# Performance work log

Hardware: AMD Instinct MI355X
Metric: run time of the kernel (lower is better)

Reference implementation:

```python
import jax, jax.numpy as jnp
import numpy as np

IN_FEATURES = 1024
OUT_FEATURES = 256
GRID_SIZE = 5
SPLINE_ORDER = 3
SCALE_BASE = 1.0
GRID_RANGE = (-1.0, 1.0)


def make_grid():
    h = (GRID_RANGE[1] - GRID_RANGE[0]) / GRID_SIZE
    g = jnp.arange(-SPLINE_ORDER, GRID_SIZE + SPLINE_ORDER + 1, dtype=jnp.float32) * h + GRID_RANGE[0]
    # (in_features, grid_size + 2*spline_order + 1) = (1024, 12)
    return jnp.broadcast_to(g[None, :], (IN_FEATURES, g.shape[0]))


def setup_inputs() -> dict:
    key = jax.random.key(0)
    k1, k2, k3 = jax.random.split(key, 3)
    batch = 16384
    x = jax.random.normal(k1, (batch, IN_FEATURES), dtype=jnp.float32)
    base_weight = jax.random.normal(k2, (OUT_FEATURES, IN_FEATURES), dtype=jnp.float32) * 0.03
    n_basis = GRID_SIZE + SPLINE_ORDER  # 8
    spline_weight = (jax.random.uniform(k3, (OUT_FEATURES, IN_FEATURES * n_basis), dtype=jnp.float32) - 0.5) * 0.1 / n_basis
    grid = make_grid()
    return {"x": x, "base_weight": base_weight, "spline_weight": spline_weight, "grid": grid}


def b_splines(x, grid):
    # x: (B, F) -> (B, F, grid_size + spline_order)
    xe = x[:, :, None]  # (B, F, 1)
    bases = ((xe >= grid[:, :-1]) & (xe < grid[:, 1:])).astype(x.dtype)
    for k in range(1, SPLINE_ORDER + 1):
        left = (xe - grid[:, : -(k + 1)]) / (grid[:, k:-1] - grid[:, : -(k + 1)])
        right = (grid[:, k + 1 :] - xe) / (grid[:, k + 1 :] - grid[:, 1:-k])
        bases = left * bases[:, :, :-1] + right * bases[:, :, 1:]
    return bases.reshape(x.shape[0], -1)  # (B, F*(grid_size+spline_order))


def reference(x, base_weight, spline_weight, grid):
    base_out = jax.nn.silu(x) @ (base_weight * SCALE_BASE).T  # (B, out)
    spline_basis = b_splines(x, grid)                          # (B, F*8)
    spline_out = spline_basis @ spline_weight.T                # (B, out)
    return base_out + spline_out
```

## Files before the change

kernel.cpp:

```cpp
#include <hip/hip_runtime.h>
#include <cstdint>
#include <cstddef>

typedef unsigned short u16;
typedef unsigned int   u32;
typedef unsigned long long u64;
typedef __attribute__((ext_vector_type(8))) short short8;
typedef __attribute__((ext_vector_type(4))) float f32x4;

#define M_ROWS 16384
#define N_COLS 256
#define IN_F   1024
#define K_SPL  8192
#define K_TOT  9216
#define NCHUNK 144
#define SPLITK 2
#define CPB    (NCHUNK / SPLITK)

__device__ __forceinline__ u32 f2bf1(float f) {
  u32 u = __float_as_uint(f);
  u += 0x7fffu + ((u >> 16) & 1u);
  return u >> 16;
}
__device__ __forceinline__ u32 pk2(float a, float b) {
  return f2bf1(a) | (f2bf1(b) << 16);
}
__device__ __forceinline__ float silu(float v) {
  return v * __builtin_amdgcn_rcpf(1.f + __expf(-v));
}

__device__ __forceinline__ uint4 basis8(float xv) {
  float u = fmaf(xv, 2.5f, 5.5f);
  int i0 = (int)u;
  float fr = u - (float)i0;
  float fr2 = fr * fr, fr3 = fr2 * fr;
  float om  = 1.f - fr;
  float om3 = om * om * om;
  float w0 = om3 * (1.f / 6.f);
  float w3 = fr3 * (1.f / 6.f);
  float w1 = fmaf(fr3, 0.5f, fmaf(fr2, -1.f, 2.f / 3.f));
  float w2 = fmaf(fr + fr2 - fr3, 0.5f, 1.f / 6.f);
  u64 W = (u64)pk2(w0, w1) | ((u64)pk2(w2, w3) << 32);
  if (!(u >= 0.f && u < 11.f)) W = 0ull;
  int s = (i0 - 3) * 16;
  u64 lo, hi;
  if (s >= 64)      { int r = s - 64; lo = 0ull; hi = (r < 64) ? (W << r) : 0ull; }
  else if (s > 0)   { lo = W << s;    hi = W >> (64 - s); }
  else if (s == 0)  { lo = W;         hi = 0ull; }
  else              { int r = -s;     lo = (r < 64) ? (W >> r) : 0ull; hi = 0ull; }
  uint4 o;
  o.x = (u32)lo; o.y = (u32)(lo >> 32); o.z = (u32)hi; o.w = (u32)(hi >> 32);
  return o;
}

__global__ void pack_weights(const float* __restrict__ bw, const float* __restrict__ sw,
                             u16* __restrict__ Bp) {
  int o  = blockIdx.y;
  int k4 = (blockIdx.x * blockDim.x + threadIdx.x) * 4;
  const float* src = (k4 < K_SPL) ? (sw + (size_t)o * K_SPL + k4)
                                  : (bw + (size_t)o * IN_F + (k4 - K_SPL));
  float a = src[0], b = src[1], c = src[2], d = src[3];
  uint2 v; v.x = pk2(a, b); v.y = pk2(c, d);
  *(uint2*)(Bp + (size_t)o * K_TOT + k4) = v;
}

__global__ __launch_bounds__(512, 4)
void kan_gemm(const float* __restrict__ x, const u16* __restrict__ Bp,
              float* __restrict__ out) {
  __shared__ __align__(16) u16 As[64 * 64];
  __shared__ __align__(16) u16 Bs[256 * 64];

  const int tid  = threadIdx.x;
  const int lane = tid & 63;
  const int w    = tid >> 6;
  const int wm   = w & 1;
  const int wn   = w >> 1;

  const int bid  = blockIdx.x;
  const int kid  = bid & 1;
  const int mb   = bid >> 1;
  const int row0 = mb * 64;
  const int cs   = kid * CPB, c1 = cs + CPB;

  f32x4 acc[2][4];
#pragma unroll
  for (int i = 0; i < 2; ++i)
#pragma unroll
    for (int j = 0; j < 4; ++j)
      acc[i][j] = (f32x4){0.f, 0.f, 0.f, 0.f};

  const int sr = tid >> 3;
  const int sq = tid & 7;

  const int lm = lane & 15;
  const int kg = lane >> 4;
  int a_off[2][2], b_off[2][4];
#pragma unroll
  for (int h = 0; h < 2; ++h) {
    int c = h * 4 + kg;
#pragma unroll
    for (int i = 0; i < 2; ++i) {
      int ra = wm * 32 + i * 16 + lm;
      a_off[h][i] = ra * 64 + ((c ^ (ra & 7)) * 8);
    }
#pragma unroll
    for (int j = 0; j < 4; ++j) {
      int rb = wn * 64 + j * 16 + lm;
      b_off[h][j] = rb * 64 + ((c ^ (rb & 7)) * 8);
    }
  }

  float px;
  float4 pb0, pb1;

  auto LOADX = [&](int c) {
    if (c < 128) {
      px = x[(size_t)(row0 + sr) * IN_F + c * 8 + sq];
    } else {
      const float* xp = x + (size_t)(row0 + sr) * IN_F + (c - 128) * 64 + sq * 8;
      pb0 = *(const float4*)xp;
      pb1 = *(const float4*)(xp + 4);
    }
  };

  auto BUILD = [&](int c) {
    uint4 q;
    if (c < 128) {
      q = basis8(px);
    } else {
      q.x = pk2(silu(pb0.x), silu(pb0.y));
      q.y = pk2(silu(pb0.z), silu(pb0.w));
      q.z = pk2(silu(pb1.x), silu(pb1.y));
      q.w = pk2(silu(pb1.z), silu(pb1.w));
    }
    *(uint4*)(As + sr * 64 + ((sq ^ (sr & 7)) * 8)) = q;
  };

  auto STAGEB = [&](int c) {
#pragma unroll
    for (int it = 0; it < 4; ++it) {
      int s = tid + it * 512;
      int r_ = s >> 3, cc = (s & 7) ^ (r_ & 7);
      const u16* gp = Bp + (size_t)r_ * K_TOT + c * 64 + cc * 8;
      __builtin_amdgcn_global_load_lds((const __attribute__((address_space(1))) void*)gp,
                                       (__attribute__((address_space(3))) void*)(Bs + s * 8),
                                       16, 0, 0);
    }
  };

  LOADX(cs);
  for (int c = cs; c < c1; ++c) {
    BUILD(c);
    STAGEB(c);
    if (c + 1 < c1) LOADX(c + 1);
    __syncthreads();
#pragma unroll
    for (int h = 0; h < 2; ++h) {
      short8 af[2], bf[4];
#pragma unroll
      for (int i = 0; i < 2; ++i) af[i] = *(const short8*)(As + a_off[h][i]);
#pragma unroll
      for (int j = 0; j < 4; ++j) bf[j] = *(const short8*)(Bs + b_off[h][j]);
#pragma unroll
      for (int i = 0; i < 2; ++i)
#pragma unroll
        for (int j = 0; j < 4; ++j)
          acc[i][j] = __builtin_amdgcn_mfma_f32_16x16x32_bf16(af[i], bf[j], acc[i][j], 0, 0, 0);
    }
    __syncthreads();
  }

  const int lc = lane & 15;
  const int lr = (lane >> 4) * 4;
#pragma unroll
  for (int i = 0; i < 2; ++i) {
#pragma unroll
    for (int j = 0; j < 4; ++j) {
      int gr = row0 + wm * 32 + i * 16 + lr;
      int gc = wn * 64 + j * 16 + lc;
      float* po = out + (size_t)gr * N_COLS + gc;
#pragma unroll
      for (int r = 0; r < 4; ++r)
        unsafeAtomicAdd(po + (size_t)r * N_COLS, acc[i][j][r]);
    }
  }
}

extern "C" void kernel_launch(void* const* d_in, const int* in_sizes, int n_in,
                              void* d_out, int out_size, void* d_ws, size_t ws_size,
                              hipStream_t stream) {
  const float* x  = (const float*)d_in[0];
  const float* bw = (const float*)d_in[1];
  const float* sw = (const float*)d_in[2];
  float* out = (float*)d_out;
  u16* Bp = (u16*)d_ws;

  hipMemsetAsync(d_out, 0, (size_t)M_ROWS * N_COLS * sizeof(float), stream);

  dim3 pgrid(K_TOT / 4 / 256, N_COLS);
  pack_weights<<<pgrid, 256, 0, stream>>>(bw, sw, Bp);

  kan_gemm<<<512, 512, 0, stream>>>(x, Bp, out);
}
```

Baseline: 212.0 us.

## Drop LDS staging: pack weights in MFMA fragment order and build A in registers

The weight pack kernel now writes bf16 weights pre-swizzled into MFMA B-fragment order, so each wave loads its B operands straight from global memory into registers. The A operands (B-spline bases and SiLU values) are computed per lane directly in registers, which removes the shared-memory tiles and both __syncthreads per chunk. Blocks drop to 256 threads (4 waves of 64 rows by 64 columns), and the loop double-buffers register loads. The split-K partition is rebalanced so one half takes spline chunks 0-71 and the other takes spline chunks 72-127 plus the base chunks. In exchange, each wave recomputes the basis values, the tile uses a large register footprint that may reduce occupancy, and there is no cross-wave reuse of B through LDS.

```diff
diff --git a/kernel.cpp b/kernel.cpp
--- a/kernel.cpp
+++ b/kernel.cpp
@@ -54,130 +54,133 @@
 }
 
 __global__ void pack_weights(const float* __restrict__ bw, const float* __restrict__ sw,
-                             u16* __restrict__ Bp) {
-  int o  = blockIdx.y;
-  int k4 = (blockIdx.x * blockDim.x + threadIdx.x) * 4;
-  const float* src = (k4 < K_SPL) ? (sw + (size_t)o * K_SPL + k4)
-                                  : (bw + (size_t)o * IN_F + (k4 - K_SPL));
-  float a = src[0], b = src[1], c = src[2], d = src[3];
-  uint2 v; v.x = pk2(a, b); v.y = pk2(c, d);
-  *(uint2*)(Bp + (size_t)o * K_TOT + k4) = v;
-}
-
-__global__ __launch_bounds__(512, 4)
-void kan_gemm(const float* __restrict__ x, const u16* __restrict__ Bp,
+                             u16* __restrict__ Bq) {
+  int t    = blockIdx.x * blockDim.x + threadIdx.x;
+  int lane = t & 63;
+  int rest = t >> 6;
+  int colf = rest & 15;
+  int hc   = rest >> 4;
+  int col  = colf * 16 + (lane & 15);
+  int kk   = (hc >> 1) * 64 + (hc & 1) * 32 + (lane >> 4) * 8;
+  const float* src = (kk < K_SPL) ? (sw + (size_t)col * K_SPL + kk)
+                                  : (bw + (size_t)col * IN_F + (kk - K_SPL));
+  uint4 v;
+  v.x = pk2(src[0], src[1]);
+  v.y = pk2(src[2], src[3]);
+  v.z = pk2(src[4], src[5]);
+  v.w = pk2(src[6], src[7]);
+  *(uint4*)(Bq + (size_t)t * 8) = v;
+}
+
+__global__ __launch_bounds__(256, 2)
+void kan_gemm(const float* __restrict__ x, const u16* __restrict__ Bq,
               float* __restrict__ out) {
-  __shared__ __align__(16) u16 As[64 * 64];
-  __shared__ __align__(16) u16 Bs[256 * 64];
-
   const int tid  = threadIdx.x;
   const int lane = tid & 63;
   const int w    = tid >> 6;
-  const int wm   = w & 1;
-  const int wn   = w >> 1;
+  const int lm   = lane & 15;
+  const int kg   = lane >> 4;
 
   const int bid  = blockIdx.x;
   const int kid  = bid & 1;
-  const int mb   = bid >> 1;
-  const int row0 = mb * 64;
-  const int cs   = kid * CPB, c1 = cs + CPB;
-
-  f32x4 acc[2][4];
-#pragma unroll
-  for (int i = 0; i < 2; ++i)
+  const int row0 = (bid >> 1) * 64;
+  const int cs   = kid * CPB;
+
+  f32x4 acc[4][4];
+#pragma unroll
+  for (int i = 0; i < 4; ++i)
 #pragma unroll
     for (int j = 0; j < 4; ++j)
       acc[i][j] = (f32x4){0.f, 0.f, 0.f, 0.f};
 
-  const int sr = tid >> 3;
-  const int sq = tid & 7;
-
-  const int lm = lane & 15;
-  const int kg = lane >> 4;
-  int a_off[2][2], b_off[2][4];
-#pragma unroll
-  for (int h = 0; h < 2; ++h) {
-    int c = h * 4 + kg;
-#pragma unroll
-    for (int i = 0; i < 2; ++i) {
-      int ra = wm * 32 + i * 16 + lm;
-      a_off[h][i] = ra * 64 + ((c ^ (ra & 7)) * 8);
-    }
-#pragma unroll
-    for (int j = 0; j < 4; ++j) {
-      int rb = wn * 64 + j * 16 + lm;
-      b_off[h][j] = rb * 64 + ((c ^ (rb & 7)) * 8);
-    }
+  const float* xr = x + (size_t)(row0 + lm) * IN_F;
+  const u16*   Bw = Bq + ((size_t)(w * 4) * 64 + lane) * 8;
+
+  auto LOADB = [&](int c, short8* bf) {
+    const u16* p = Bw + (size_t)c * (32 * 512);
+#pragma unroll
+    for (int h = 0; h < 2; ++h)
+#pragma unroll
+      for (int j = 0; j < 4; ++j)
+        bf[h * 4 + j] = *(const short8*)(p + (h * 16 + j) * 512);
+  };
+
+  auto LXS = [&](int c, float* pxv) {
+#pragma unroll
+    for (int i = 0; i < 4; ++i) {
+      const float* p = xr + i * (16 * IN_F) + c * 8 + kg;
+      pxv[i * 2 + 0] = p[0];
+      pxv[i * 2 + 1] = p[4];
+    }
+  };
+
+  auto SPL = [&](const float* pxv, const short8* bf) {
+#pragma unroll
+    for (int h = 0; h < 2; ++h) {
+      short8 af[4];
+#pragma unroll
+      for (int i = 0; i < 4; ++i) {
+        uint4 q = basis8(pxv[i * 2 + h]);
+        af[i] = *(const short8*)&q;
+      }
+#pragma unroll
+      for (int i = 0; i < 4; ++i)
+#pragma unroll
+        for (int j = 0; j < 4; ++j)
+          acc[i][j] = __builtin_amdgcn_mfma_f32_16x16x32_bf16(af[i], bf[h * 4 + j], acc[i][j], 0, 0, 0);
+    }
+  };
+
+  auto BASEC = [&](int c, const short8* bf) {
+#pragma unroll
+    for (int h = 0; h < 2; ++h)
+#pragma unroll
+      for (int i = 0; i < 4; ++i) {
+        const float* p = xr + i * (16 * IN_F) + (c - 128) * 64 + h * 32 + kg * 8;
+        float4 a  = *(const float4*)p;
+        float4 b2 = *(const float4*)(p + 4);
+        uint4 q;
+        q.x = pk2(silu(a.x),  silu(a.y));
+        q.y = pk2(silu(a.z),  silu(a.w));
+        q.z = pk2(silu(b2.x), silu(b2.y));
+        q.w = pk2(silu(b2.z), silu(b2.w));
+        short8 af = *(const short8*)&q;
+#pragma unroll
+        for (int j = 0; j < 4; ++j)
+          acc[i][j] = __builtin_amdgcn_mfma_f32_16x16x32_bf16(af, bf[h * 4 + j], acc[i][j], 0, 0, 0);
+      }
+  };
+
+  float  pxA[8], pxB[8];
+  short8 bfA[8], bfB[8];
+
+  const int se = kid ? 128 : 72;
+  LXS(cs, pxA); LOADB(cs, bfA);
+  for (int c = cs; c < se; c += 2) {
+    LXS(c + 1, pxB); LOADB(c + 1, bfB);
+    SPL(pxA, bfA);
+    if (c + 2 < se) { LXS(c + 2, pxA); LOADB(c + 2, bfA); }
+    SPL(pxB, bfB);
   }
 
-  float px;
-  float4 pb0, pb1;
-
-  auto LOADX = [&](int c) {
-    if (c < 128) {
-      px = x[(size_t)(row0 + sr) * IN_F + c * 8 + sq];
-    } else {
-      const float* xp = x + (size_t)(row0 + sr) * IN_F + (c - 128) * 64 + sq * 8;
-      pb0 = *(const float4*)xp;
-      pb1 = *(const float4*)(xp + 4);
-    }
-  };
-
-  auto BUILD = [&](int c) {
-    uint4 q;
-    if (c < 128) {
-      q = basis8(px);
-    } else {
-      q.x = pk2(silu(pb0.x), silu(pb0.y));
-      q.y = pk2(silu(pb0.z), silu(pb0.w));
-      q.z = pk2(silu(pb1.x), silu(pb1.y));
-      q.w = pk2(silu(pb1.z), silu(pb1.w));
-    }
-    *(uint4*)(As + sr * 64 + ((sq ^ (sr & 7)) * 8)) = q;
-  };
-
-  auto STAGEB = [&](int c) {
-#pragma unroll
-    for (int it = 0; it < 4; ++it) {
-      int s = tid + it * 512;
-      int r_ = s >> 3, cc = (s & 7) ^ (r_ & 7);
-      const u16* gp = Bp + (size_t)r_ * K_TOT + c * 64 + cc * 8;
-      __builtin_amdgcn_global_load_lds((const __attribute__((address_space(1))) void*)gp,
-                                       (__attribute__((address_space(3))) void*)(Bs + s * 8),
-                                       16, 0, 0);
-    }
-  };
-
-  LOADX(cs);
-  for (int c = cs; c < c1; ++c) {
-    BUILD(c);
-    STAGEB(c);
-    if (c + 1 < c1) LOADX(c + 1);
-    __syncthreads();
-#pragma unroll
-    for (int h = 0; h < 2; ++h) {
-      short8 af[2], bf[4];
-#pragma unroll
-      for (int i = 0; i < 2; ++i) af[i] = *(const short8*)(As + a_off[h][i]);
-#pragma unroll
-      for (int j = 0; j < 4; ++j) bf[j] = *(const short8*)(Bs + b_off[h][j]);
-#pragma unroll
-      for (int i = 0; i < 2; ++i)
-#pragma unroll
-        for (int j = 0; j < 4; ++j)
-          acc[i][j] = __builtin_amdgcn_mfma_f32_16x16x32_bf16(af[i], bf[j], acc[i][j], 0, 0, 0);
-    }
-    __syncthreads();
+  if (kid) {
+    LOADB(128, bfA);
+    for (int c = 128; c < 144; c += 2) {
+      LOADB(c + 1, bfB);
+      BASEC(c, bfA);
+      if (c + 2 < 144) LOADB(c + 2, bfA);
+      BASEC(c + 1, bfB);
+    }
   }
 
   const int lc = lane & 15;
   const int lr = (lane >> 4) * 4;
 #pragma unroll
-  for (int i = 0; i < 2; ++i) {
+  for (int i = 0; i < 4; ++i) {
 #pragma unroll
     for (int j = 0; j < 4; ++j) {
-      int gr = row0 + wm * 32 + i * 16 + lr;
-      int gc = wn * 64 + j * 16 + lc;
+      int gr = row0 + i * 16 + lr;
+      int gc = w * 64 + j * 16 + lc;
       float* po = out + (size_t)gr * N_COLS + gc;
 #pragma unroll
       for (int r = 0; r < 4; ++r)
@@ -193,12 +196,11 @@
   const float* bw = (const float*)d_in[1];
   const float* sw = (const float*)d_in[2];
   float* out = (float*)d_out;
-  u16* Bp = (u16*)d_ws;
+  u16* Bq = (u16*)d_ws;
 
   hipMemsetAsync(d_out, 0, (size_t)M_ROWS * N_COLS * sizeof(float), stream);
 
-  dim3 pgrid(K_TOT / 4 / 256, N_COLS);
-  pack_weights<<<pgrid, 256, 0, stream>>>(bw, sw, Bp);
-
-  kan_gemm<<<512, 512, 0, stream>>>(x, Bp, out);
-}
+  pack_weights<<<1152, 256, 0, stream>>>(bw, sw, Bq);
+
+  kan_gemm<<<512, 256, 0, stream>>>(x, Bq, out);
+}
```

After: 300.2 us. +41.6%, slower.
